# Kernel tuning notes

Hardware: AMD Instinct MI355X
Metric: run time of the kernel (lower is better)

Reference implementation:

```python
import jax, jax.numpy as jnp
import numpy as np

N, E, H, F, G, L = 20000, 320000, 128, 128, 50, 6
CUTOFF = 5.0
LOG2 = 0.6931471805599453  # shift of ShiftedSoftplus
PI = np.pi


def ssp(x):
    # ShiftedSoftplus: softplus(x) - log(2)
    return jax.nn.softplus(x) - LOG2


def setup_inputs() -> dict:
    key = jax.random.key(0)
    ks = jax.random.split(key, 12)
    v = jax.random.normal(ks[0], (N, H), jnp.float32)
    pos = jax.random.uniform(ks[1], (N, 3), jnp.float32) * 2.0
    offsets_real = jax.random.normal(ks[2], (E, 3), jnp.float32) * 0.3
    edges = jax.random.randint(ks[3], (2, E), 0, N, jnp.int32)
    s = lambda k, shp, fan_in: jax.random.normal(k, shp, jnp.float32) / np.sqrt(fan_in)
    # update_e params (torch Linear weights stored as [in, out] for x @ W)
    lin_w = s(ks[4], (L, H, F), H)        # Linear(hidden, filters, bias=False)
    w1 = s(ks[5], (L, G, F), G)           # mlp[0]: Linear(gaussians, filters)
    b1 = jnp.zeros((L, F), jnp.float32)
    w2 = s(ks[6], (L, F, F), F)           # mlp[2]: Linear(filters, filters)
    b2 = jnp.zeros((L, F), jnp.float32)
    # update_v params
    u1 = s(ks[7], (L, F, H), F)           # lin1: Linear(filters, hidden)
    ub1 = jnp.zeros((L, H), jnp.float32)
    u2 = s(ks[8], (L, H, H), H)           # lin2: Linear(hidden, hidden)
    ub2 = jnp.zeros((L, H), jnp.float32)
    return {"v": v, "pos": pos, "offsets_real": offsets_real, "edges": edges,
            "lin_w": lin_w, "w1": w1, "b1": b1, "w2": w2, "b2": b2,
            "u1": u1, "ub1": ub1, "u2": u2, "ub2": ub2}


def reference(v, pos, offsets_real, edges, lin_w, w1, b1, w2, b2, u1, ub1, u2, ub2):
    row, col = edges[0], edges[1]
    # pairwise distances with periodic offsets: [E]
    diff = pos[col] + offsets_real - pos[row]
    dist = jnp.sqrt(jnp.sum(diff * diff, axis=-1))
    # Gaussian RBF expansion: [E, G]
    offset = jnp.linspace(0.0, CUTOFF, G)
    coeff = -0.5 / (offset[1] - offset[0]) ** 2
    demb = jnp.exp(coeff * (dist[:, None] - offset[None, :]) ** 2)
    # cosine cutoff envelope: [E]
    C = 0.5 * (jnp.cos(dist * PI / CUTOFF) + 1.0)
    for l in range(L):
        # continuous filter from RBFs: [E, F]
        Wf = (ssp(demb @ w1[l] + b1[l]) @ w2[l] + b2[l]) * C[:, None]
        # update_e: project nodes then gather source features
        e = (v @ lin_w[l])[row] * Wf                      # [E, F]
        # update_v: scatter-add messages to targets, residual MLP
        agg = jax.ops.segment_sum(e, col, num_segments=N)  # [N, F]
        out = ssp(agg @ u1[l] + ub1[l]) @ u2[l] + ub2[l]
        v = v + out
    return v
```

## Files before the change

### kernel.cpp

```cpp
#include <hip/hip_runtime.h>
#include <hip/hip_bf16.h>
#include <math.h>

#define HH 128
#define FF 128
#define GG 50
#define NLAYERS 6
#define NPB 16
#define TAB 16384
#define TABH 4.8828125e-4f
#define TABINVH 2048.0f
#define SCB 32
#define DP 16

typedef __attribute__((ext_vector_type(8))) short bf16x8;
typedef __attribute__((ext_vector_type(4))) float f32x4;

static __device__ __forceinline__ float ssp(float x) {
    return fmaxf(x, 0.f) + __logf(1.f + __expf(-fabsf(x))) - 0.6931471805599453f;
}

static __device__ __forceinline__ short f2bf(float x) {
    union { float f; unsigned u; } c; c.f = x;
    unsigned r = (c.u + 0x7FFF + ((c.u >> 16) & 1)) >> 16;
    return (short)r;
}

static __device__ __forceinline__ float bf2f_lo(unsigned p) {
    union { unsigned u; float f; } c; c.u = p << 16; return c.f;
}
static __device__ __forceinline__ float bf2f_hi(unsigned p) {
    union { unsigned u; float f; } c; c.u = p & 0xFFFF0000u; return c.f;
}

__global__ void hist_kernel(const int* __restrict__ col, int* __restrict__ counts, int E_) {
    int e = blockIdx.x * 256 + threadIdx.x;
    if (e < E_) atomicAdd(&counts[col[e]], 1);
}

__global__ __launch_bounds__(1024) void pscan1_kernel(const int* __restrict__ counts,
                                                      int* __restrict__ psum, int N_) {
    __shared__ int wsum[16];
    const int tid = threadIdx.x;
    const int lane = tid & 63, wid = tid >> 6;
    const int chunk = (N_ + SCB - 1) / SCB;
    int i = blockIdx.x * chunk + tid;
    int val = (tid < chunk && i < N_) ? counts[i] : 0;
#pragma unroll
    for (int d = 1; d < 64; d <<= 1) val += __shfl_xor(val, d, 64);
    if (lane == 0) wsum[wid] = val;
    __syncthreads();
    if (wid == 0) {
        int s = (lane < 16) ? wsum[lane] : 0;
#pragma unroll
        for (int d = 1; d < 16; d <<= 1) s += __shfl_xor(s, d, 64);
        if (lane == 0) psum[blockIdx.x] = s;
    }
}

__global__ void pscan2_kernel(const int* __restrict__ psum, int* __restrict__ pbase) {
    const int tid = threadIdx.x;
    int v = (tid < SCB) ? psum[tid] : 0;
    int x = v;
#pragma unroll
    for (int d = 1; d < 64; d <<= 1) {
        int t = __shfl_up(x, d, 64);
        if (tid >= d) x += t;
    }
    if (tid < SCB) pbase[tid] = x - v;
}

__global__ __launch_bounds__(1024) void pscan3_kernel(const int* __restrict__ counts,
                                                      const int* __restrict__ pbase,
                                                      int* __restrict__ offsets,
                                                      int* __restrict__ woff, int N_) {
    __shared__ int wsum[16];
    const int tid = threadIdx.x;
    const int lane = tid & 63, wid = tid >> 6;
    const int chunk = (N_ + SCB - 1) / SCB;
    int i = blockIdx.x * chunk + tid;
    int val = (tid < chunk && i < N_) ? counts[i] : 0;
    int x = val;
#pragma unroll
    for (int d = 1; d < 64; d <<= 1) {
        int t = __shfl_up(x, d, 64);
        if (lane >= d) x += t;
    }
    if (lane == 63) wsum[wid] = x;
    __syncthreads();
    if (wid == 0) {
        int s = (lane < 16) ? wsum[lane] : 0;
#pragma unroll
        for (int d = 1; d < 16; d <<= 1) {
            int t = __shfl_up(s, d, 64);
            if (lane >= d) s += t;
        }
        if (lane < 16) wsum[lane] = s;
    }
    __syncthreads();
    int woffset = (wid > 0) ? wsum[wid - 1] : 0;
    if (tid < chunk && i < N_) {
        int ex = pbase[blockIdx.x] + woffset + x - val;
        offsets[i] = ex;
        woff[i] = ex;
    }
}

__global__ void scatter_kernel(const float* __restrict__ pos,
                               const float* __restrict__ offs,
                               const int* __restrict__ row,
                               const int* __restrict__ col,
                               int* __restrict__ woff,
                               int* __restrict__ meta, int E_) {
    int e = blockIdx.x * 256 + threadIdx.x;
    if (e >= E_) return;
    int r = row[e], c = col[e];
    float dx = pos[c * 3 + 0] + offs[e * 3 + 0] - pos[r * 3 + 0];
    float dy = pos[c * 3 + 1] + offs[e * 3 + 1] - pos[r * 3 + 1];
    float dz = pos[c * 3 + 2] + offs[e * 3 + 2] - pos[r * 3 + 2];
    float d = sqrtf(dx * dx + dy * dy + dz * dz);
    int ix = (int)(d * TABINVH + 0.5f);
    if (ix > TAB - 1) ix = TAB - 1;
    int p = atomicAdd(&woff[c], 1);
    meta[p] = r | (ix << 17);
}

__global__ __launch_bounds__(256) void prep_kernel(
    const float* __restrict__ w1, const float* __restrict__ w2,
    const float* __restrict__ u1, const float* __restrict__ u2,
    const float* __restrict__ lin_w,
    short* __restrict__ w1t, short* __restrict__ w2t,
    short* __restrict__ u1t, short* __restrict__ u2t, short* __restrict__ lin_wt) {
    int idx = blockIdx.x * 256 + threadIdx.x;
    if (idx < NLAYERS * FF * FF) {
        int l = idx >> 14, r = idx & 16383, a = r >> 7, b = r & 127;
        size_t src = (size_t)l * FF * FF + (size_t)b * FF + a;
        w2t[idx] = f2bf(w2[src]);
        u1t[idx] = f2bf(u1[src]);
        u2t[idx] = f2bf(u2[src]);
        lin_wt[idx] = f2bf(lin_w[src]);
    }
    if (idx < NLAYERS * FF * 64) {
        int l = idx >> 13, r = idx & 8191, fo = r >> 6, g = r & 63;
        w1t[idx] = f2bf(g < GG ? w1[((size_t)l * GG + g) * FF + fo] : 0.f);
    }
}

__global__ __launch_bounds__(256) void vproj0_kernel(const float* __restrict__ vb,
                                                     const short* __restrict__ lwt,
                                                     unsigned short* __restrict__ out,
                                                     int N_) {
    const int tid = threadIdx.x;
    const int lane = tid & 63, wave = tid >> 6;
    const int l15 = lane & 15, l4 = lane >> 4;
    const int n0 = wave * 32;
    const int nb0 = blockIdx.x * 64;
    bf16x8 bw[2][4];
#pragma unroll
    for (int n = 0; n < 2; n++)
#pragma unroll
        for (int ks = 0; ks < 4; ks++)
            bw[n][ks] = *(const bf16x8*)&lwt[(n0 + n * 16 + l15) * 128 + ks * 32 + l4 * 8];
#pragma unroll
    for (int m = 0; m < 4; m++) {
        f32x4 acc0 = {0.f, 0.f, 0.f, 0.f}, acc1 = {0.f, 0.f, 0.f, 0.f};
        int arow = nb0 + m * 16 + l15;
        const float* ap = &vb[(size_t)(arow < N_ ? arow : 0) * HH];
#pragma unroll
        for (int ks = 0; ks < 4; ks++) {
            float4 x0 = *(const float4*)&ap[ks * 32 + l4 * 8];
            float4 x1 = *(const float4*)&ap[ks * 32 + l4 * 8 + 4];
            bf16x8 a = {f2bf(x0.x), f2bf(x0.y), f2bf(x0.z), f2bf(x0.w),
                        f2bf(x1.x), f2bf(x1.y), f2bf(x1.z), f2bf(x1.w)};
            acc0 = __builtin_amdgcn_mfma_f32_16x16x32_bf16(a, bw[0][ks], acc0, 0, 0, 0);
            acc1 = __builtin_amdgcn_mfma_f32_16x16x32_bf16(a, bw[1][ks], acc1, 0, 0, 0);
        }
#pragma unroll
        for (int r = 0; r < 4; r++) {
            int gn = nb0 + m * 16 + l4 * 4 + r;
            if (gn < N_) {
                out[(size_t)gn * FF + n0 + l15] = (unsigned short)f2bf(acc0[r]);
                out[(size_t)gn * FF + n0 + 16 + l15] = (unsigned short)f2bf(acc1[r]);
            }
        }
    }
}

__global__ __launch_bounds__(256) void tab_kernel(
    const short* __restrict__ w1t, const float* __restrict__ b1,
    const short* __restrict__ w2t, const float* __restrict__ b2,
    unsigned short* __restrict__ tab) {
    __shared__ __align__(16) short h1_s[64 * 136];
    const int tid = threadIdx.x;
    const int lane = tid & 63, wave = tid >> 6;
    const int l15 = lane & 15, l4 = lane >> 4;
    const int n0w = wave * 32;
    const int l = blockIdx.x / (TAB / 64);
    const int tb0 = (blockIdx.x % (TAB / 64)) * 64;
    const short* w1l = w1t + (size_t)l * FF * 64;
    const short* w2l = w2t + (size_t)l * FF * FF;
    unsigned short* tabl = tab + (size_t)l * TAB * FF;

    bf16x8 bw1[2][2], bw2[2][4];
    float bias1[2], bias2[2];
#pragma unroll
    for (int n = 0; n < 2; n++) {
        const int fo = n0w + n * 16 + l15;
        bias1[n] = b1[(size_t)l * FF + fo];
        bias2[n] = b2[(size_t)l * FF + fo];
#pragma unroll
        for (int ks = 0; ks < 2; ks++)
            bw1[n][ks] = *(const bf16x8*)&w1l[fo * 64 + ks * 32 + l4 * 8];
#pragma unroll
        for (int ks = 0; ks < 4; ks++)
            bw2[n][ks] = *(const bf16x8*)&w2l[fo * 128 + ks * 32 + l4 * 8];
    }

    const float STEP = 5.0f / 49.0f;
    const float COEFF = -0.5f / (STEP * STEP);
#pragma unroll
    for (int m = 0; m < 4; m++) {
        float d = (float)(tb0 + m * 16 + l15) * TABH;
        bf16x8 a0, a1;
#pragma unroll
        for (int j = 0; j < 8; j++) {
            int g0 = l4 * 8 + j;
            float x0 = fmaf((float)g0, -STEP, d);
            a0[j] = f2bf(__expf(COEFF * x0 * x0));
            int g1 = 32 + l4 * 8 + j;
            float x1 = fmaf((float)g1, -STEP, d);
            a1[j] = (g1 < GG) ? f2bf(__expf(COEFF * x1 * x1)) : (short)0;
        }
#pragma unroll
        for (int n = 0; n < 2; n++) {
            f32x4 acc = {bias1[n], bias1[n], bias1[n], bias1[n]};
            acc = __builtin_amdgcn_mfma_f32_16x16x32_bf16(a0, bw1[n][0], acc, 0, 0, 0);
            acc = __builtin_amdgcn_mfma_f32_16x16x32_bf16(a1, bw1[n][1], acc, 0, 0, 0);
            const int f = n0w + n * 16 + l15;
#pragma unroll
            for (int r = 0; r < 4; r++)
                h1_s[(m * 16 + l4 * 4 + r) * 136 + f] = f2bf(ssp(acc[r]));
        }
    }
    __syncthreads();

#pragma unroll
    for (int m = 0; m < 4; m++) {
        f32x4 accA = {bias2[0], bias2[0], bias2[0], bias2[0]};
        f32x4 accB = {bias2[1], bias2[1], bias2[1], bias2[1]};
#pragma unroll
        for (int ks = 0; ks < 4; ks++) {
            bf16x8 a = *(const bf16x8*)&h1_s[(m * 16 + l15) * 136 + ks * 32 + l4 * 8];
            accA = __builtin_amdgcn_mfma_f32_16x16x32_bf16(a, bw2[0][ks], accA, 0, 0, 0);
            accB = __builtin_amdgcn_mfma_f32_16x16x32_bf16(a, bw2[1][ks], accB, 0, 0, 0);
        }
#pragma unroll
        for (int r = 0; r < 4; r++) {
            int entry = tb0 + m * 16 + l4 * 4 + r;
            float de = (float)entry * TABH;
            float C = 0.5f * (cosf(de * 0.6283185307179586f) + 1.0f);
            tabl[(size_t)entry * FF + n0w + l15] = (unsigned short)f2bf(accA[r] * C);
            tabl[(size_t)entry * FF + n0w + 16 + l15] = (unsigned short)f2bf(accB[r] * C);
        }
    }
}

__global__ __launch_bounds__(512) void layer_kernel(
    const int* __restrict__ meta,
    const int* __restrict__ off_start, const int* __restrict__ off_end,
    const unsigned* __restrict__ tab, const unsigned* __restrict__ vin,
    const short* __restrict__ u1t, const float* __restrict__ ub1,
    const short* __restrict__ u2t, const float* __restrict__ ub2,
    float* __restrict__ vb, const short* __restrict__ lwt_next,
    unsigned short* __restrict__ vout, int N_) {
    __shared__ __align__(16) float agg_s[NPB * 132];
    __shared__ __align__(16) short t1_s[NPB * 136];
    short* t2_s = (short*)agg_s;

    const int tid = threadIdx.x;
    const int lane = tid & 63, wave = tid >> 6;
    const int l15 = lane & 15, l4 = lane >> 4;
    const int n0c = wave * 16;
    const int nb0 = blockIdx.x * NPB;

#pragma unroll
    for (int s = 0; s < 2; s++) {
        const int nl = wave * 2 + s;
        const int n = nb0 + nl;
        float acc0 = 0.f, acc1 = 0.f;
        if (n < N_) {
            const int e0 = __builtin_amdgcn_readfirstlane(off_start[n]);
            const int e1 = __builtin_amdgcn_readfirstlane(off_end[n]);
            if (e1 > e0) {
                int mmn[DP];
#pragma unroll
                for (int j = 0; j < DP; j++) {
                    int e = e0 + j; if (e >= e1) e = e1 - 1;
                    mmn[j] = meta[e];
                }
                for (int base = e0; base < e1; base += DP) {
                    int mw[DP];
#pragma unroll
                    for (int j = 0; j < DP; j++)
                        mw[j] = __builtin_amdgcn_readfirstlane(mmn[j]);
                    unsigned tp[DP], vp[DP];
#pragma unroll
                    for (int j = 0; j < DP; j++) {
                        const int r_ = mw[j] & 0x1ffff;
                        const int ix = (int)((unsigned)mw[j] >> 17);
                        tp[j] = tab[(size_t)ix * 64 + lane];
                        vp[j] = vin[(size_t)r_ * 64 + lane];
                    }
                    const int nb2 = base + DP;
                    if (nb2 < e1) {
#pragma unroll
                        for (int j = 0; j < DP; j++) {
                            int e = nb2 + j; if (e >= e1) e = e1 - 1;
                            mmn[j] = meta[e];
                        }
                    }
#pragma unroll
                    for (int j = 0; j < DP; j++) {
                        if (base + j < e1) {
                            acc0 = fmaf(bf2f_lo(tp[j]), bf2f_lo(vp[j]), acc0);
                            acc1 = fmaf(bf2f_hi(tp[j]), bf2f_hi(vp[j]), acc1);
                        }
                    }
                }
            }
        }
        agg_s[nl * 132 + 2 * lane] = acc0;
        agg_s[nl * 132 + 2 * lane + 1] = acc1;
    }
    __syncthreads();

    {
        bf16x8 bw[4];
        const float bias = ub1[n0c + l15];
#pragma unroll
        for (int ks = 0; ks < 4; ks++)
            bw[ks] = *(const bf16x8*)&u1t[(n0c + l15) * 128 + ks * 32 + l4 * 8];
        const float* ap = &agg_s[l15 * 132];
        f32x4 acc = {bias, bias, bias, bias};
#pragma unroll
        for (int ks = 0; ks < 4; ks++) {
            float4 x0 = *(const float4*)&ap[ks * 32 + l4 * 8];
            float4 x1 = *(const float4*)&ap[ks * 32 + l4 * 8 + 4];
            bf16x8 a = {f2bf(x0.x), f2bf(x0.y), f2bf(x0.z), f2bf(x0.w),
                        f2bf(x1.x), f2bf(x1.y), f2bf(x1.z), f2bf(x1.w)};
            acc = __builtin_amdgcn_mfma_f32_16x16x32_bf16(a, bw[ks], acc, 0, 0, 0);
        }
#pragma unroll
        for (int r = 0; r < 4; r++) {
            int er = l4 * 4 + r;
            t1_s[er * 136 + n0c + l15] = f2bf(ssp(acc[r]));
        }
    }
    __syncthreads();

    {
        bf16x8 bw[4];
        const float bias = ub2[n0c + l15];
#pragma unroll
        for (int ks = 0; ks < 4; ks++)
            bw[ks] = *(const bf16x8*)&u2t[(n0c + l15) * 128 + ks * 32 + l4 * 8];
        f32x4 acc = {bias, bias, bias, bias};
#pragma unroll
        for (int ks = 0; ks < 4; ks++) {
            bf16x8 a = *(const bf16x8*)&t1_s[(l15) * 136 + ks * 32 + l4 * 8];
            acc = __builtin_amdgcn_mfma_f32_16x16x32_bf16(a, bw[ks], acc, 0, 0, 0);
        }
        __syncthreads();
#pragma unroll
        for (int r = 0; r < 4; r++) {
            int er = l4 * 4 + r;
            int gn = nb0 + er;
            if (gn < N_) {
                size_t i0 = (size_t)gn * HH + n0c + l15;
                float v0 = vb[i0] + acc[r];
                vb[i0] = v0;
                t2_s[er * 136 + n0c + l15] = f2bf(v0);
            } else {
                t2_s[er * 136 + n0c + l15] = 0;
            }
        }
    }
    __syncthreads();

    if (lwt_next) {
        bf16x8 bw[4];
#pragma unroll
        for (int ks = 0; ks < 4; ks++)
            bw[ks] = *(const bf16x8*)&lwt_next[(n0c + l15) * 128 + ks * 32 + l4 * 8];
        f32x4 acc = {0.f, 0.f, 0.f, 0.f};
#pragma unroll
        for (int ks = 0; ks < 4; ks++) {
            bf16x8 a = *(const bf16x8*)&t2_s[(l15) * 136 + ks * 32 + l4 * 8];
            acc = __builtin_amdgcn_mfma_f32_16x16x32_bf16(a, bw[ks], acc, 0, 0, 0);
        }
#pragma unroll
        for (int r = 0; r < 4; r++) {
            int gn = nb0 + l4 * 4 + r;
            if (gn < N_) {
                vout[(size_t)gn * FF + n0c + l15] = (unsigned short)f2bf(acc[r]);
            }
        }
    }
}

extern "C" void kernel_launch(void* const* d_in, const int* in_sizes, int n_in,
                              void* d_out, int out_size, void* d_ws, size_t ws_size,
                              hipStream_t stream) {
    const float* v = (const float*)d_in[0];
    const float* pos = (const float*)d_in[1];
    const float* offs = (const float*)d_in[2];
    const int* edges = (const int*)d_in[3];
    const float* lin_w = (const float*)d_in[4];
    const float* w1 = (const float*)d_in[5];
    const float* b1 = (const float*)d_in[6];
    const float* w2 = (const float*)d_in[7];
    const float* b2 = (const float*)d_in[8];
    const float* u1 = (const float*)d_in[9];
    const float* ub1 = (const float*)d_in[10];
    const float* u2 = (const float*)d_in[11];
    const float* ub2 = (const float*)d_in[12];

    const int N = in_sizes[0] / HH;
    const int E = in_sizes[3] / 2;
    const int* row = edges;
    const int* col = edges + E;

    char* base = (char*)d_ws;
    int* counts = (int*)base;    base += (size_t)N * 4;
    int* woff = (int*)base;      base += (size_t)N * 4;
    int* offsets = (int*)base;   base += (size_t)N * 4;
    int* psum = (int*)base;      base += (size_t)SCB * 4;
    int* pbase = (int*)base;     base += (size_t)SCB * 4 + 24;
    int* meta = (int*)base;      base += (size_t)E * 4;
    unsigned short* vprojA = (unsigned short*)base; base += (size_t)N * FF * 2;
    unsigned short* vprojB = (unsigned short*)base; base += (size_t)N * FF * 2;
    short* w1t = (short*)base;   base += (size_t)NLAYERS * FF * 64 * 2;
    short* w2t = (short*)base;   base += (size_t)NLAYERS * FF * FF * 2;
    short* u1t = (short*)base;   base += (size_t)NLAYERS * FF * FF * 2;
    short* u2t = (short*)base;   base += (size_t)NLAYERS * FF * FF * 2;
    short* lin_wt = (short*)base; base += (size_t)NLAYERS * FF * FF * 2;
    unsigned short* tab = (unsigned short*)base;

    float* vbuf = (float*)d_out;

    const int EB = (E + 255) / 256;
    const int NB64 = (N + 63) / 64;
    const int NBn = (N + NPB - 1) / NPB;

    hipMemsetAsync(counts, 0, (size_t)N * 4, stream);
    hist_kernel<<<EB, 256, 0, stream>>>(col, counts, E);
    pscan1_kernel<<<SCB, 1024, 0, stream>>>(counts, psum, N);
    pscan2_kernel<<<1, 64, 0, stream>>>(psum, pbase);
    pscan3_kernel<<<SCB, 1024, 0, stream>>>(counts, pbase, offsets, woff, N);
    scatter_kernel<<<EB, 256, 0, stream>>>(pos, offs, row, col, woff, meta, E);
    prep_kernel<<<(NLAYERS * FF * FF + 255) / 256, 256, 0, stream>>>(
        w1, w2, u1, u2, lin_w, w1t, w2t, u1t, u2t, lin_wt);
    tab_kernel<<<NLAYERS * (TAB / 64), 256, 0, stream>>>(w1t, b1, w2t, b2, tab);
    hipMemcpyAsync(vbuf, v, (size_t)N * HH * sizeof(float),
                   hipMemcpyDeviceToDevice, stream);
    vproj0_kernel<<<NB64, 256, 0, stream>>>(v, lin_wt, vprojA, N);

    for (int l = 0; l < NLAYERS; l++) {
        unsigned short* vin = (l & 1) ? vprojB : vprojA;
        unsigned short* vout = (l & 1) ? vprojA : vprojB;
        layer_kernel<<<NBn, 512, 0, stream>>>(
            meta, offsets, woff, (const unsigned*)(tab + (size_t)l * TAB * FF),
            (const unsigned*)vin,
            u1t + (size_t)l * FF * FF, ub1 + (size_t)l * HH,
            u2t + (size_t)l * FF * FF, ub2 + (size_t)l * HH, vbuf,
            (l + 1 < NLAYERS) ? (lin_wt + (size_t)(l + 1) * FF * FF) : nullptr,
            vout, N);
    }
}
```

Baseline: 302.1 us.

## Halve filter table, fuse v copy into vproj0, merge two-node edge loops

Halves the distance lookup table resolution (8192 entries) to shrink the table build and its cache footprint. Folds the device-to-device copy of v into vproj0_kernel so one launch and one pass over v disappear. Each wave now walks the edges of its two consecutive nodes in one combined loop, splitting the accumulators at the node boundary. This fills the 16-wide edge batches better but adds a per-edge branch. The coarser table also lowers the accuracy of the filter interpolation.

```diff
diff --git a/kernel.cpp b/kernel.cpp
--- a/kernel.cpp
+++ b/kernel.cpp
@@ -7,9 +7,9 @@
 #define GG 50
 #define NLAYERS 6
 #define NPB 16
-#define TAB 16384
-#define TABH 4.8828125e-4f
-#define TABINVH 2048.0f
+#define TAB 8192
+#define TABH 9.765625e-4f
+#define TABINVH 1024.0f
 #define SCB 32
 #define DP 16
 
@@ -149,12 +149,20 @@
 __global__ __launch_bounds__(256) void vproj0_kernel(const float* __restrict__ vb,
                                                      const short* __restrict__ lwt,
                                                      unsigned short* __restrict__ out,
+                                                     float* __restrict__ vbuf_out,
                                                      int N_) {
     const int tid = threadIdx.x;
     const int lane = tid & 63, wave = tid >> 6;
     const int l15 = lane & 15, l4 = lane >> 4;
     const int n0 = wave * 32;
     const int nb0 = blockIdx.x * 64;
+    for (int i = tid; i < 64 * 32; i += 256) {
+        int r = i >> 5, c = i & 31;
+        int gn = nb0 + r;
+        if (gn < N_)
+            *(float4*)&vbuf_out[(size_t)gn * HH + c * 4] =
+                *(const float4*)&vb[(size_t)gn * HH + c * 4];
+    }
     bf16x8 bw[2][4];
 #pragma unroll
     for (int n = 0; n < 2; n++)
@@ -283,14 +291,14 @@
     const int n0c = wave * 16;
     const int nb0 = blockIdx.x * NPB;
 
-#pragma unroll
-    for (int s = 0; s < 2; s++) {
-        const int nl = wave * 2 + s;
-        const int n = nb0 + nl;
-        float acc0 = 0.f, acc1 = 0.f;
-        if (n < N_) {
-            const int e0 = __builtin_amdgcn_readfirstlane(off_start[n]);
-            const int e1 = __builtin_amdgcn_readfirstlane(off_end[n]);
+    {
+        const int nA = nb0 + wave * 2;
+        const int nB = nA + 1;
+        float a0A = 0.f, a1A = 0.f, a0B = 0.f, a1B = 0.f;
+        if (nA < N_) {
+            const int e0 = __builtin_amdgcn_readfirstlane(off_start[nA]);
+            const int bnd = __builtin_amdgcn_readfirstlane(off_end[nA]);
+            const int e1 = (nB < N_) ? __builtin_amdgcn_readfirstlane(off_end[nB]) : bnd;
             if (e1 > e0) {
                 int mmn[DP];
 #pragma unroll
@@ -321,16 +329,27 @@
                     }
 #pragma unroll
                     for (int j = 0; j < DP; j++) {
-                        if (base + j < e1) {
-                            acc0 = fmaf(bf2f_lo(tp[j]), bf2f_lo(vp[j]), acc0);
-                            acc1 = fmaf(bf2f_hi(tp[j]), bf2f_hi(vp[j]), acc1);
+                        const int e = base + j;
+                        if (e < e1) {
+                            const float w0 = bf2f_lo(tp[j]);
+                            const float w1 = bf2f_hi(tp[j]);
+                            if (e < bnd) {
+                                a0A = fmaf(w0, bf2f_lo(vp[j]), a0A);
+                                a1A = fmaf(w1, bf2f_hi(vp[j]), a1A);
+                            } else {
+                                a0B = fmaf(w0, bf2f_lo(vp[j]), a0B);
+                                a1B = fmaf(w1, bf2f_hi(vp[j]), a1B);
+                            }
                         }
                     }
                 }
             }
         }
-        agg_s[nl * 132 + 2 * lane] = acc0;
-        agg_s[nl * 132 + 2 * lane + 1] = acc1;
+        const int nl = wave * 2;
+        agg_s[nl * 132 + 2 * lane] = a0A;
+        agg_s[nl * 132 + 2 * lane + 1] = a1A;
+        agg_s[(nl + 1) * 132 + 2 * lane] = a0B;
+        agg_s[(nl + 1) * 132 + 2 * lane + 1] = a1B;
     }
     __syncthreads();
 
@@ -461,9 +480,7 @@
     prep_kernel<<<(NLAYERS * FF * FF + 255) / 256, 256, 0, stream>>>(
         w1, w2, u1, u2, lin_w, w1t, w2t, u1t, u2t, lin_wt);
     tab_kernel<<<NLAYERS * (TAB / 64), 256, 0, stream>>>(w1t, b1, w2t, b2, tab);
-    hipMemcpyAsync(vbuf, v, (size_t)N * HH * sizeof(float),
-                   hipMemcpyDeviceToDevice, stream);
-    vproj0_kernel<<<NB64, 256, 0, stream>>>(v, lin_wt, vprojA, N);
+    vproj0_kernel<<<NB64, 256, 0, stream>>>(v, lin_wt, vprojA, vbuf, N);
 
     for (int l = 0; l < NLAYERS; l++) {
         unsigned short* vin = (l & 1) ? vprojB : vprojA;
```

After: 342.3 us. +13.3%, slower.
